# Kernel optimization log

Measured on AMD Instinct MI355X. Metric: run time of the kernel, lower is better.

## Reference

```python
import jax, jax.numpy as jnp
import numpy as np

NUM_CLASSES = 100
TEMPERATURE = 0.7
EPS = 1e-8  # F.cosine_similarity default eps
N, D = 8192, 256


def setup_inputs() -> dict:
    key = jax.random.key(0)
    k1, k2 = jax.random.split(key)
    fusion_feature = jax.random.normal(k1, (N, D), dtype=jnp.float32)
    labels = jax.random.randint(k2, (N,), 0, NUM_CLASSES, dtype=jnp.int64)
    return {"fusion_feature": fusion_feature, "labels": labels}


def reference(fusion_feature, labels):
    n = fusion_feature.shape[0]
    # --- label-grouped mean prototypes (scatter-mean by label) ---
    sums = jax.ops.segment_sum(fusion_feature, labels, num_segments=NUM_CLASSES)
    counts = jax.ops.segment_sum(jnp.ones((n,), fusion_feature.dtype), labels,
                                 num_segments=NUM_CLASSES)
    proto = sums / jnp.maximum(counts, 1.0)[:, None]   # [C, D]
    u = proto[labels]                                   # [n, D] prototype per sample
    # --- cosine similarity matrix [n, n] (torch eps-clamped norms) ---
    f_norm = jnp.maximum(jnp.linalg.norm(fusion_feature, axis=1), EPS)  # [n]
    u_norm = jnp.maximum(jnp.linalg.norm(u, axis=1), EPS)               # [n]
    sim = (fusion_feature @ u.T) / (f_norm[:, None] * u_norm[None, :])  # [n, n]
    # --- contrastive reduction ---
    e = jnp.exp(sim / TEMPERATURE)
    row_sum = jnp.sum(e, axis=1)          # denominator over all prototypes
    diag = jnp.diagonal(e)                # numerator: own prototype
    loss = jnp.sum(-jnp.log(diag / row_sum)) / n
    return loss
```

## Files before the change

### kernel.cpp

```cpp
#include <hip/hip_runtime.h>

#define NROWS 8192
#define DIM 256
#define NCLS 100
#define NCLS_PAD 128
#define TEMP 0.7f
#define EPSV 1e-8f
#define LMAX 512

typedef __attribute__((ext_vector_type(8))) short short8;
typedef __attribute__((ext_vector_type(4))) float f32x4;

static __device__ __forceinline__ unsigned short f2bf(float x) {
    unsigned u = __builtin_bit_cast(unsigned, x);
    return (unsigned short)((u + 0x7FFFu + ((u >> 16) & 1u)) >> 16);
}

__global__ __launch_bounds__(512) void k_proto(const float* __restrict__ f,
                                               const int* __restrict__ labels,
                                               unsigned short* __restrict__ protoB,
                                               float* __restrict__ countf,
                                               float* __restrict__ out) {
    int c = blockIdx.x, tid = threadIdx.x;
    __shared__ int list[LMAX];
    __shared__ int nm;
    __shared__ float4 red4[512];
    if (tid == 0) nm = 0;
    __syncthreads();
    int lv[16];
    #pragma unroll
    for (int i = 0; i < 16; ++i) lv[i] = labels[i * 512 + tid];
    #pragma unroll
    for (int i = 0; i < 16; ++i)
        if (lv[i] == c) {
            int idx = atomicAdd(&nm, 1);
            if (idx < LMAX) list[idx] = i * 512 + tid;
        }
    __syncthreads();
    int n = nm < LMAX ? nm : LMAX;
    int g = tid >> 6, d = tid & 63;
    float4 acc = make_float4(0.f, 0.f, 0.f, 0.f);
    int i = g;
    for (; i + 32 <= n; i += 32) {
        float4 v0 = *(const float4*)&f[list[i +  0] * DIM + d * 4];
        float4 v1 = *(const float4*)&f[list[i +  8] * DIM + d * 4];
        float4 v2 = *(const float4*)&f[list[i + 16] * DIM + d * 4];
        float4 v3 = *(const float4*)&f[list[i + 24] * DIM + d * 4];
        acc.x += (v0.x + v1.x) + (v2.x + v3.x);
        acc.y += (v0.y + v1.y) + (v2.y + v3.y);
        acc.z += (v0.z + v1.z) + (v2.z + v3.z);
        acc.w += (v0.w + v1.w) + (v2.w + v3.w);
    }
    for (; i + 16 <= n; i += 16) {
        float4 v0 = *(const float4*)&f[list[i + 0] * DIM + d * 4];
        float4 v1 = *(const float4*)&f[list[i + 8] * DIM + d * 4];
        acc.x += v0.x + v1.x; acc.y += v0.y + v1.y;
        acc.z += v0.z + v1.z; acc.w += v0.w + v1.w;
    }
    for (; i < n; i += 8) {
        float4 v = *(const float4*)&f[list[i] * DIM + d * 4];
        acc.x += v.x; acc.y += v.y; acc.z += v.z; acc.w += v.w;
    }
    red4[tid] = acc;
    __syncthreads();
    if (tid < 64) {
        float4 s = red4[d];
        #pragma unroll
        for (int k = 1; k < 8; ++k) {
            float4 t = red4[d + 64 * k];
            s.x += t.x; s.y += t.y; s.z += t.z; s.w += t.w;
        }
        float invn = 1.0f / fmaxf((float)n, 1.0f);
        float mx = s.x * invn, my = s.y * invn, mz = s.z * invn, mw = s.w * invn;
        float ssq = mx * mx + my * my + mz * mz + mw * mw;
        #pragma unroll
        for (int m = 32; m > 0; m >>= 1) ssq += __shfl_xor(ssq, m);
        float scale = 1.0f / (fmaxf(sqrtf(ssq), EPSV) * TEMP);
        ushort4 o;
        o.x = f2bf(mx * scale);
        o.y = f2bf(my * scale);
        o.z = f2bf(mz * scale);
        o.w = f2bf(mw * scale);
        *(ushort4*)&protoB[c * DIM + d * 4] = o;
        if (d == 0) {
            countf[c] = (float)n;
            if (c == NCLS_PAD - 1) out[0] = 0.0f;
        }
    }
}

__global__ __launch_bounds__(256) void k_main(const float* __restrict__ f,
                                              const int* __restrict__ labels,
                                              const unsigned short* __restrict__ protoB,
                                              const float* __restrict__ countf,
                                              float* __restrict__ out) {
    int tid = threadIdx.x;
    int rb = blockIdx.x * 16;
    __shared__ unsigned short As[16 * DIM];
    __shared__ float invfS[16];
    __shared__ float dgS[16];
    __shared__ float wsum[4][16];
    char* asb = (char*)As;

    {
        int row = tid >> 4, s = tid & 15;
        const float* fr = f + (rb + row) * DIM;
        float4 v[4];
        #pragma unroll
        for (int i = 0; i < 4; ++i) v[i] = *(const float4*)(fr + (s + 16 * i) * 4);
        float ss = 0.f;
        #pragma unroll
        for (int i = 0; i < 4; ++i) {
            ss += v[i].x * v[i].x + v[i].y * v[i].y + v[i].z * v[i].z + v[i].w * v[i].w;
            ushort4 o;
            o.x = f2bf(v[i].x); o.y = f2bf(v[i].y); o.z = f2bf(v[i].z); o.w = f2bf(v[i].w);
            int byte = (row * 512 + s * 8 + i * 128) ^ ((row & 7) << 4);
            *(ushort4*)(asb + byte) = o;
        }
        ss += __shfl_xor(ss, 1); ss += __shfl_xor(ss, 2);
        ss += __shfl_xor(ss, 4); ss += __shfl_xor(ss, 8);
        if (s == 0) invfS[row] = 1.0f / fmaxf(sqrtf(ss), EPSV);
    }
    __syncthreads();

    int w = tid >> 6, l = tid & 63;
    int n16 = l & 15, q = l >> 4;
    f32x4 acc0 = {0.f, 0.f, 0.f, 0.f}, acc1 = {0.f, 0.f, 0.f, 0.f};
    const unsigned short* pb0 = protoB + ((2 * w)     * 16 + n16) * DIM + q * 8;
    const unsigned short* pb1 = protoB + ((2 * w + 1) * 16 + n16) * DIM + q * 8;
    int arow = n16 * 512 + q * 16;
    int swz  = (n16 & 7) << 4;
    #pragma unroll
    for (int kc = 0; kc < DIM; kc += 32) {
        short8 af = *(const short8*)(asb + ((arow + kc * 2) ^ swz));
        short8 b0 = *(const short8*)(pb0 + kc);
        short8 b1 = *(const short8*)(pb1 + kc);
        acc0 = __builtin_amdgcn_mfma_f32_16x16x32_bf16(af, b0, acc0, 0, 0, 0);
        acc1 = __builtin_amdgcn_mfma_f32_16x16x32_bf16(af, b1, acc1, 0, 0, 0);
    }

    int lab4[4];
    float inv4[4];
    #pragma unroll
    for (int j = 0; j < 4; ++j) {
        lab4[j] = labels[rb + q * 4 + j];
        inv4[j] = invfS[q * 4 + j];
    }
    int col0 = n16 + 16 * (2 * w);
    int col1 = col0 + 16;
    float cf0 = countf[col0], cf1 = countf[col1];
    float rp[4];
    #pragma unroll
    for (int j = 0; j < 4; ++j) {
        float a0 = acc0[j] * inv4[j];
        float a1 = acc1[j] * inv4[j];
        rp[j] = cf0 * __expf(a0) + cf1 * __expf(a1);
        if (col0 == lab4[j]) dgS[q * 4 + j] = a0;
        if (col1 == lab4[j]) dgS[q * 4 + j] = a1;
    }
    #pragma unroll
    for (int m = 1; m <= 8; m <<= 1) {
        #pragma unroll
        for (int j = 0; j < 4; ++j) rp[j] += __shfl_xor(rp[j], m);
    }
    if (n16 == 0) {
        #pragma unroll
        for (int j = 0; j < 4; ++j) wsum[w][q * 4 + j] = rp[j];
    }
    __syncthreads();
    if (tid < 16) {
        float tot = wsum[0][tid] + wsum[1][tid] + wsum[2][tid] + wsum[3][tid];
        float v = __logf(tot) - dgS[tid];
        v += __shfl_xor(v, 1); v += __shfl_xor(v, 2);
        v += __shfl_xor(v, 4); v += __shfl_xor(v, 8);
        if (tid == 0) atomicAdd(out, v * (1.0f / (float)NROWS));
    }
}

extern "C" void kernel_launch(void* const* d_in, const int* in_sizes, int n_in,
                              void* d_out, int out_size, void* d_ws, size_t ws_size,
                              hipStream_t stream) {
    const float* f      = (const float*)d_in[0];
    const int*   labels = (const int*)d_in[1];
    unsigned short* protoB = (unsigned short*)d_ws;
    float* countf          = (float*)d_ws + 16384;

    k_proto<<<NCLS_PAD, 512, 0, stream>>>(f, labels, protoB, countf, (float*)d_out);
    k_main<<<NROWS / 16, 256, 0, stream>>>(f, labels, protoB, countf, (float*)d_out);
}
```

Measured before the change: 74.98 us.

## Fuse prototype and main kernels into one cooperative launch with grid sync

Merges the prototype-building kernel and the similarity/loss kernel into a single cooperative kernel of 512 blocks. The first 128 blocks also compute the class prototypes, and every block stages its own row tile and norms before a grid-wide barrier, then all blocks run the MFMA and reduction phase. The aim is to remove the second launch and overlap the row staging with prototype construction. The grid sync adds its own barrier cost and requires all 512 blocks to be co-resident, which is why it falls back to the two-kernel path if the cooperative launch fails.

```diff
diff --git a/kernel.cpp b/kernel.cpp
--- a/kernel.cpp
+++ b/kernel.cpp
@@ -1,4 +1,7 @@
 #include <hip/hip_runtime.h>
+#include <hip/hip_cooperative_groups.h>
+
+namespace cg = cooperative_groups;
 
 #define NROWS 8192
 #define DIM 256
@@ -14,6 +17,159 @@
 static __device__ __forceinline__ unsigned short f2bf(float x) {
     unsigned u = __builtin_bit_cast(unsigned, x);
     return (unsigned short)((u + 0x7FFFu + ((u >> 16) & 1u)) >> 16);
+}
+
+__global__ __launch_bounds__(256, 2) void k_fused(const float* __restrict__ f,
+                                                  const int* __restrict__ labels,
+                                                  unsigned short* __restrict__ protoB,
+                                                  float* __restrict__ countf,
+                                                  float* __restrict__ out) {
+    int tid = threadIdx.x, bid = blockIdx.x;
+    int rb = bid * 16;
+    __shared__ unsigned short As[16 * DIM];
+    __shared__ float invfS[16];
+    __shared__ float dgS[16];
+    __shared__ float wsum[4][16];
+    __shared__ int list[LMAX];
+    __shared__ int nm;
+    __shared__ float4 red4[256];
+    char* asb = (char*)As;
+
+    bool isproto = bid < NCLS_PAD;
+    if (tid == 0) nm = 0;
+
+    int lv[32];
+    if (isproto) {
+        #pragma unroll
+        for (int i = 0; i < 32; ++i) lv[i] = labels[i * 256 + tid];
+    }
+
+    {
+        int row = tid >> 4, s = tid & 15;
+        const float* fr = f + (rb + row) * DIM;
+        float4 v[4];
+        #pragma unroll
+        for (int i = 0; i < 4; ++i) v[i] = *(const float4*)(fr + (s + 16 * i) * 4);
+        float ss = 0.f;
+        #pragma unroll
+        for (int i = 0; i < 4; ++i) {
+            ss += v[i].x * v[i].x + v[i].y * v[i].y + v[i].z * v[i].z + v[i].w * v[i].w;
+            ushort4 o;
+            o.x = f2bf(v[i].x); o.y = f2bf(v[i].y); o.z = f2bf(v[i].z); o.w = f2bf(v[i].w);
+            int byte = (row * 512 + s * 8 + i * 128) ^ ((row & 7) << 4);
+            *(ushort4*)(asb + byte) = o;
+        }
+        ss += __shfl_xor(ss, 1); ss += __shfl_xor(ss, 2);
+        ss += __shfl_xor(ss, 4); ss += __shfl_xor(ss, 8);
+        if (s == 0) invfS[row] = 1.0f / fmaxf(sqrtf(ss), EPSV);
+    }
+
+    if (isproto) {
+        int c = bid;
+        __syncthreads();
+        #pragma unroll
+        for (int i = 0; i < 32; ++i)
+            if (lv[i] == c) {
+                int idx = atomicAdd(&nm, 1);
+                if (idx < LMAX) list[idx] = i * 256 + tid;
+            }
+        __syncthreads();
+        int n = nm < LMAX ? nm : LMAX;
+        int g = tid >> 6, d = tid & 63;
+        float4 acc = make_float4(0.f, 0.f, 0.f, 0.f);
+        int i = g;
+        for (; i + 16 <= n; i += 16) {
+            float4 v0 = *(const float4*)&f[list[i +  0] * DIM + d * 4];
+            float4 v1 = *(const float4*)&f[list[i +  4] * DIM + d * 4];
+            float4 v2 = *(const float4*)&f[list[i +  8] * DIM + d * 4];
+            float4 v3 = *(const float4*)&f[list[i + 12] * DIM + d * 4];
+            acc.x += (v0.x + v1.x) + (v2.x + v3.x);
+            acc.y += (v0.y + v1.y) + (v2.y + v3.y);
+            acc.z += (v0.z + v1.z) + (v2.z + v3.z);
+            acc.w += (v0.w + v1.w) + (v2.w + v3.w);
+        }
+        for (; i < n; i += 4) {
+            float4 v = *(const float4*)&f[list[i] * DIM + d * 4];
+            acc.x += v.x; acc.y += v.y; acc.z += v.z; acc.w += v.w;
+        }
+        red4[tid] = acc;
+        __syncthreads();
+        if (tid < 64) {
+            float4 s0 = red4[d], s1 = red4[d + 64], s2 = red4[d + 128], s3 = red4[d + 192];
+            float invn = 1.0f / fmaxf((float)n, 1.0f);
+            float mx = (s0.x + s1.x + s2.x + s3.x) * invn;
+            float my = (s0.y + s1.y + s2.y + s3.y) * invn;
+            float mz = (s0.z + s1.z + s2.z + s3.z) * invn;
+            float mw = (s0.w + s1.w + s2.w + s3.w) * invn;
+            float ssq = mx * mx + my * my + mz * mz + mw * mw;
+            #pragma unroll
+            for (int m = 32; m > 0; m >>= 1) ssq += __shfl_xor(ssq, m);
+            float scale = 1.0f / (fmaxf(sqrtf(ssq), EPSV) * TEMP);
+            ushort4 o;
+            o.x = f2bf(mx * scale);
+            o.y = f2bf(my * scale);
+            o.z = f2bf(mz * scale);
+            o.w = f2bf(mw * scale);
+            *(ushort4*)&protoB[c * DIM + d * 4] = o;
+            if (d == 0) countf[c] = (float)n;
+        }
+        if (bid == 0 && tid == 0) out[0] = 0.0f;
+        __threadfence();
+    }
+    cg::this_grid().sync();
+
+    int w = tid >> 6, l = tid & 63;
+    int n16 = l & 15, q = l >> 4;
+    f32x4 acc0 = {0.f, 0.f, 0.f, 0.f}, acc1 = {0.f, 0.f, 0.f, 0.f};
+    const unsigned short* pb0 = protoB + ((2 * w)     * 16 + n16) * DIM + q * 8;
+    const unsigned short* pb1 = protoB + ((2 * w + 1) * 16 + n16) * DIM + q * 8;
+    int arow = n16 * 512 + q * 16;
+    int swz  = (n16 & 7) << 4;
+    #pragma unroll
+    for (int kc = 0; kc < DIM; kc += 32) {
+        short8 af = *(const short8*)(asb + ((arow + kc * 2) ^ swz));
+        short8 b0 = *(const short8*)(pb0 + kc);
+        short8 b1 = *(const short8*)(pb1 + kc);
+        acc0 = __builtin_amdgcn_mfma_f32_16x16x32_bf16(af, b0, acc0, 0, 0, 0);
+        acc1 = __builtin_amdgcn_mfma_f32_16x16x32_bf16(af, b1, acc1, 0, 0, 0);
+    }
+
+    int lab4[4];
+    float inv4[4];
+    #pragma unroll
+    for (int j = 0; j < 4; ++j) {
+        lab4[j] = labels[rb + q * 4 + j];
+        inv4[j] = invfS[q * 4 + j];
+    }
+    int col0 = n16 + 16 * (2 * w);
+    int col1 = col0 + 16;
+    float cf0 = countf[col0], cf1 = countf[col1];
+    float rp[4];
+    #pragma unroll
+    for (int j = 0; j < 4; ++j) {
+        float a0 = acc0[j] * inv4[j];
+        float a1 = acc1[j] * inv4[j];
+        rp[j] = cf0 * __expf(a0) + cf1 * __expf(a1);
+        if (col0 == lab4[j]) dgS[q * 4 + j] = a0;
+        if (col1 == lab4[j]) dgS[q * 4 + j] = a1;
+    }
+    #pragma unroll
+    for (int m = 1; m <= 8; m <<= 1) {
+        #pragma unroll
+        for (int j = 0; j < 4; ++j) rp[j] += __shfl_xor(rp[j], m);
+    }
+    if (n16 == 0) {
+        #pragma unroll
+        for (int j = 0; j < 4; ++j) wsum[w][q * 4 + j] = rp[j];
+    }
+    __syncthreads();
+    if (tid < 16) {
+        float tot = wsum[0][tid] + wsum[1][tid] + wsum[2][tid] + wsum[3][tid];
+        float v = __logf(tot) - dgS[tid];
+        v += __shfl_xor(v, 1); v += __shfl_xor(v, 2);
+        v += __shfl_xor(v, 4); v += __shfl_xor(v, 8);
+        if (tid == 0) atomicAdd(out, v * (1.0f / (float)NROWS));
+    }
 }
 
 __global__ __launch_bounds__(512) void k_proto(const float* __restrict__ f,
@@ -51,12 +207,6 @@
         acc.z += (v0.z + v1.z) + (v2.z + v3.z);
         acc.w += (v0.w + v1.w) + (v2.w + v3.w);
     }
-    for (; i + 16 <= n; i += 16) {
-        float4 v0 = *(const float4*)&f[list[i + 0] * DIM + d * 4];
-        float4 v1 = *(const float4*)&f[list[i + 8] * DIM + d * 4];
-        acc.x += v0.x + v1.x; acc.y += v0.y + v1.y;
-        acc.z += v0.z + v1.z; acc.w += v0.w + v1.w;
-    }
     for (; i < n; i += 8) {
         float4 v = *(const float4*)&f[list[i] * DIM + d * 4];
         acc.x += v.x; acc.y += v.y; acc.z += v.z; acc.w += v.w;
@@ -77,10 +227,8 @@
         for (int m = 32; m > 0; m >>= 1) ssq += __shfl_xor(ssq, m);
         float scale = 1.0f / (fmaxf(sqrtf(ssq), EPSV) * TEMP);
         ushort4 o;
-        o.x = f2bf(mx * scale);
-        o.y = f2bf(my * scale);
-        o.z = f2bf(mz * scale);
-        o.w = f2bf(mw * scale);
+        o.x = f2bf(mx * scale); o.y = f2bf(my * scale);
+        o.z = f2bf(mz * scale); o.w = f2bf(mw * scale);
         *(ushort4*)&protoB[c * DIM + d * 4] = o;
         if (d == 0) {
             countf[c] = (float)n;
@@ -101,7 +249,6 @@
     __shared__ float dgS[16];
     __shared__ float wsum[4][16];
     char* asb = (char*)As;
-
     {
         int row = tid >> 4, s = tid & 15;
         const float* fr = f + (rb + row) * DIM;
@@ -122,7 +269,6 @@
         if (s == 0) invfS[row] = 1.0f / fmaxf(sqrtf(ss), EPSV);
     }
     __syncthreads();
-
     int w = tid >> 6, l = tid & 63;
     int n16 = l & 15, q = l >> 4;
     f32x4 acc0 = {0.f, 0.f, 0.f, 0.f}, acc1 = {0.f, 0.f, 0.f, 0.f};
@@ -138,7 +284,6 @@
         acc0 = __builtin_amdgcn_mfma_f32_16x16x32_bf16(af, b0, acc0, 0, 0, 0);
         acc1 = __builtin_amdgcn_mfma_f32_16x16x32_bf16(af, b1, acc1, 0, 0, 0);
     }
-
     int lab4[4];
     float inv4[4];
     #pragma unroll
@@ -184,7 +329,15 @@
     const int*   labels = (const int*)d_in[1];
     unsigned short* protoB = (unsigned short*)d_ws;
     float* countf          = (float*)d_ws + 16384;
-
-    k_proto<<<NCLS_PAD, 512, 0, stream>>>(f, labels, protoB, countf, (float*)d_out);
-    k_main<<<NROWS / 16, 256, 0, stream>>>(f, labels, protoB, countf, (float*)d_out);
-}
+    float* outp            = (float*)d_out;
+
+    void* args[] = { (void*)&f, (void*)&labels, (void*)&protoB, (void*)&countf,
+                     (void*)&outp };
+    hipError_t e = hipLaunchCooperativeKernel(reinterpret_cast<void*>(k_fused),
+                                              dim3(NROWS / 16), dim3(256),
+                                              args, 0, stream);
+    if (e != hipSuccess) {
+        k_proto<<<NCLS_PAD, 512, 0, stream>>>(f, labels, protoB, countf, outp);
+        k_main<<<NROWS / 16, 256, 0, stream>>>(f, labels, protoB, countf, outp);
+    }
+}
```

New measurement: 150.0 us. +100.0%, slower.

## Move feature bf16 conversion and norms into the prototype kernel's extra blocks

Applied to the files above, without the earlier changes.

The per-row fp32 to bf16 conversion, swizzling and inverse-norm computation move out of the main kernel into additional blocks of the first kernel, so they run alongside the per-class prototype reduction. The main kernel then only copies a pre-swizzled bf16 tile and reads precomputed inverse norms. The prototype blocks shrink from 512 to 256 threads with a matching unroll. In exchange the change adds a workspace round trip of the bf16 features (4 MB written, then read back), and the main kernel now depends on the first kernel for more of its data.

```diff
diff --git a/kernel.cpp b/kernel.cpp
--- a/kernel.cpp
+++ b/kernel.cpp
@@ -16,62 +16,81 @@
     return (unsigned short)((u + 0x7FFFu + ((u >> 16) & 1u)) >> 16);
 }
 
-__global__ __launch_bounds__(512) void k_proto(const float* __restrict__ f,
-                                               const int* __restrict__ labels,
-                                               unsigned short* __restrict__ protoB,
-                                               float* __restrict__ countf,
-                                               float* __restrict__ out) {
-    int c = blockIdx.x, tid = threadIdx.x;
+__global__ __launch_bounds__(256) void k_prep(const float* __restrict__ f,
+                                              const int* __restrict__ labels,
+                                              unsigned short* __restrict__ protoB,
+                                              float* __restrict__ countf,
+                                              float* __restrict__ invf,
+                                              unsigned short* __restrict__ fbf,
+                                              float* __restrict__ out) {
+    int tid = threadIdx.x, bid = blockIdx.x;
     __shared__ int list[LMAX];
     __shared__ int nm;
-    __shared__ float4 red4[512];
+    __shared__ float4 red4[256];
+
+    if (bid >= NCLS_PAD) {
+        int tb = bid - NCLS_PAD;
+        int row = tid >> 4, s = tid & 15;
+        const float* fr = f + (tb * 16 + row) * DIM;
+        char* tile = (char*)fbf + tb * 8192;
+        float4 v[4];
+        #pragma unroll
+        for (int i = 0; i < 4; ++i) v[i] = *(const float4*)(fr + (s + 16 * i) * 4);
+        float ss = 0.f;
+        #pragma unroll
+        for (int i = 0; i < 4; ++i) {
+            ss += v[i].x * v[i].x + v[i].y * v[i].y + v[i].z * v[i].z + v[i].w * v[i].w;
+            ushort4 o;
+            o.x = f2bf(v[i].x); o.y = f2bf(v[i].y); o.z = f2bf(v[i].z); o.w = f2bf(v[i].w);
+            int byte = (row * 512 + s * 8 + i * 128) ^ ((row & 7) << 4);
+            *(ushort4*)(tile + byte) = o;
+        }
+        ss += __shfl_xor(ss, 1); ss += __shfl_xor(ss, 2);
+        ss += __shfl_xor(ss, 4); ss += __shfl_xor(ss, 8);
+        if (s == 0) invf[tb * 16 + row] = 1.0f / fmaxf(sqrtf(ss), EPSV);
+        return;
+    }
+
+    int c = bid;
     if (tid == 0) nm = 0;
-    __syncthreads();
-    int lv[16];
-    #pragma unroll
-    for (int i = 0; i < 16; ++i) lv[i] = labels[i * 512 + tid];
-    #pragma unroll
-    for (int i = 0; i < 16; ++i)
+    int lv[32];
+    #pragma unroll
+    for (int i = 0; i < 32; ++i) lv[i] = labels[i * 256 + tid];
+    __syncthreads();
+    #pragma unroll
+    for (int i = 0; i < 32; ++i)
         if (lv[i] == c) {
             int idx = atomicAdd(&nm, 1);
-            if (idx < LMAX) list[idx] = i * 512 + tid;
+            if (idx < LMAX) list[idx] = i * 256 + tid;
         }
     __syncthreads();
     int n = nm < LMAX ? nm : LMAX;
     int g = tid >> 6, d = tid & 63;
     float4 acc = make_float4(0.f, 0.f, 0.f, 0.f);
     int i = g;
-    for (; i + 32 <= n; i += 32) {
+    for (; i + 16 <= n; i += 16) {
         float4 v0 = *(const float4*)&f[list[i +  0] * DIM + d * 4];
-        float4 v1 = *(const float4*)&f[list[i +  8] * DIM + d * 4];
-        float4 v2 = *(const float4*)&f[list[i + 16] * DIM + d * 4];
-        float4 v3 = *(const float4*)&f[list[i + 24] * DIM + d * 4];
+        float4 v1 = *(const float4*)&f[list[i +  4] * DIM + d * 4];
+        float4 v2 = *(const float4*)&f[list[i +  8] * DIM + d * 4];
+        float4 v3 = *(const float4*)&f[list[i + 12] * DIM + d * 4];
         acc.x += (v0.x + v1.x) + (v2.x + v3.x);
         acc.y += (v0.y + v1.y) + (v2.y + v3.y);
         acc.z += (v0.z + v1.z) + (v2.z + v3.z);
         acc.w += (v0.w + v1.w) + (v2.w + v3.w);
     }
-    for (; i + 16 <= n; i += 16) {
-        float4 v0 = *(const float4*)&f[list[i + 0] * DIM + d * 4];
-        float4 v1 = *(const float4*)&f[list[i + 8] * DIM + d * 4];
-        acc.x += v0.x + v1.x; acc.y += v0.y + v1.y;
-        acc.z += v0.z + v1.z; acc.w += v0.w + v1.w;
-    }
-    for (; i < n; i += 8) {
+    for (; i < n; i += 4) {
         float4 v = *(const float4*)&f[list[i] * DIM + d * 4];
         acc.x += v.x; acc.y += v.y; acc.z += v.z; acc.w += v.w;
     }
     red4[tid] = acc;
     __syncthreads();
     if (tid < 64) {
-        float4 s = red4[d];
-        #pragma unroll
-        for (int k = 1; k < 8; ++k) {
-            float4 t = red4[d + 64 * k];
-            s.x += t.x; s.y += t.y; s.z += t.z; s.w += t.w;
-        }
+        float4 s0 = red4[d], s1 = red4[d + 64], s2 = red4[d + 128], s3 = red4[d + 192];
         float invn = 1.0f / fmaxf((float)n, 1.0f);
-        float mx = s.x * invn, my = s.y * invn, mz = s.z * invn, mw = s.w * invn;
+        float mx = (s0.x + s1.x + s2.x + s3.x) * invn;
+        float my = (s0.y + s1.y + s2.y + s3.y) * invn;
+        float mz = (s0.z + s1.z + s2.z + s3.z) * invn;
+        float mw = (s0.w + s1.w + s2.w + s3.w) * invn;
         float ssq = mx * mx + my * my + mz * mz + mw * mw;
         #pragma unroll
         for (int m = 32; m > 0; m >>= 1) ssq += __shfl_xor(ssq, m);
@@ -82,44 +101,32 @@
         o.z = f2bf(mz * scale);
         o.w = f2bf(mw * scale);
         *(ushort4*)&protoB[c * DIM + d * 4] = o;
-        if (d == 0) {
-            countf[c] = (float)n;
-            if (c == NCLS_PAD - 1) out[0] = 0.0f;
-        }
-    }
-}
-
-__global__ __launch_bounds__(256) void k_main(const float* __restrict__ f,
-                                              const int* __restrict__ labels,
+        if (d == 0) countf[c] = (float)n;
+    }
+    if (bid == 0 && tid == 0) out[0] = 0.0f;
+}
+
+__global__ __launch_bounds__(256) void k_main(const int* __restrict__ labels,
                                               const unsigned short* __restrict__ protoB,
                                               const float* __restrict__ countf,
+                                              const float* __restrict__ invf,
+                                              const unsigned short* __restrict__ fbf,
                                               float* __restrict__ out) {
     int tid = threadIdx.x;
     int rb = blockIdx.x * 16;
-    __shared__ unsigned short As[16 * DIM];
+    __shared__ __align__(16) unsigned short As[16 * DIM];
     __shared__ float invfS[16];
     __shared__ float dgS[16];
     __shared__ float wsum[4][16];
     char* asb = (char*)As;
 
     {
-        int row = tid >> 4, s = tid & 15;
-        const float* fr = f + (rb + row) * DIM;
-        float4 v[4];
-        #pragma unroll
-        for (int i = 0; i < 4; ++i) v[i] = *(const float4*)(fr + (s + 16 * i) * 4);
-        float ss = 0.f;
-        #pragma unroll
-        for (int i = 0; i < 4; ++i) {
-            ss += v[i].x * v[i].x + v[i].y * v[i].y + v[i].z * v[i].z + v[i].w * v[i].w;
-            ushort4 o;
-            o.x = f2bf(v[i].x); o.y = f2bf(v[i].y); o.z = f2bf(v[i].z); o.w = f2bf(v[i].w);
-            int byte = (row * 512 + s * 8 + i * 128) ^ ((row & 7) << 4);
-            *(ushort4*)(asb + byte) = o;
-        }
-        ss += __shfl_xor(ss, 1); ss += __shfl_xor(ss, 2);
-        ss += __shfl_xor(ss, 4); ss += __shfl_xor(ss, 8);
-        if (s == 0) invfS[row] = 1.0f / fmaxf(sqrtf(ss), EPSV);
+        const char* src = (const char*)fbf + blockIdx.x * 8192 + tid * 16;
+        short8 a = *(const short8*)src;
+        short8 b = *(const short8*)(src + 4096);
+        *(short8*)(asb + tid * 16) = a;
+        *(short8*)(asb + tid * 16 + 4096) = b;
+        if (tid < 16) invfS[tid] = invf[rb + tid];
     }
     __syncthreads();
 
@@ -183,8 +190,12 @@
     const float* f      = (const float*)d_in[0];
     const int*   labels = (const int*)d_in[1];
     unsigned short* protoB = (unsigned short*)d_ws;
-    float* countf          = (float*)d_ws + 16384;
-
-    k_proto<<<NCLS_PAD, 512, 0, stream>>>(f, labels, protoB, countf, (float*)d_out);
-    k_main<<<NROWS / 16, 256, 0, stream>>>(f, labels, protoB, countf, (float*)d_out);
-}
+    float* countf          = (float*)((char*)d_ws + 65536);
+    float* invf            = (float*)((char*)d_ws + 66048);
+    unsigned short* fbf    = (unsigned short*)((char*)d_ws + 131072);
+    float* outp            = (float*)d_out;
+
+    k_prep<<<NCLS_PAD + NROWS / 16, 256, 0, stream>>>(f, labels, protoB, countf,
+                                                      invf, fbf, outp);
+    k_main<<<NROWS / 16, 256, 0, stream>>>(labels, protoB, countf, invf, fbf, outp);
+}
```

Result: slower. 79.29 us (+5.7%).
